# Optimization experiments

Hardware: AMD Instinct MI355X
Metric: run time of the kernel (lower is better)

The kernel has to match this reference:

```python
import jax, jax.numpy as jnp
import numpy as np

N, DEG, D, L = 20000, 32, 128, 2
EPS = 1e-7
MAX_TANH_ARG = 1.0 - 1e-5


def _logmap0(x, sqrt_c):
    # Poincare ball log map at the origin: artanh(sqrt(c)||x||) * x / (sqrt(c)||x||)
    norm = jnp.maximum(jnp.linalg.norm(x, axis=-1, keepdims=True), EPS)
    arg = jnp.minimum(sqrt_c * norm, MAX_TANH_ARG)
    return jnp.arctanh(arg) * x / (sqrt_c * norm)


def _expmap0(v, sqrt_c):
    # Poincare ball exp map at the origin: tanh(sqrt(c)||v||) * v / (sqrt(c)||v||)
    norm = jnp.maximum(jnp.linalg.norm(v, axis=-1, keepdims=True), EPS)
    return jnp.tanh(sqrt_c * norm) * v / (sqrt_c * norm)


def setup_inputs() -> dict:
    key = jax.random.key(0)
    ks = jax.random.split(key, 7)
    neighbors = jax.random.randint(ks[0], (N, DEG), 0, N)  # fixed in-degree predecessor lists
    node_embeddings = jax.random.normal(ks[1], (N, D), dtype=jnp.float32)
    in_proj_w = jax.random.normal(ks[2], (L, 3 * D, D), dtype=jnp.float32) * 0.02
    in_proj_b = jax.random.normal(ks[3], (L, 3 * D), dtype=jnp.float32) * 0.02
    out_proj_w = jax.random.normal(ks[4], (L, D, D), dtype=jnp.float32) * 0.02
    out_proj_b = jax.random.normal(ks[5], (L, D), dtype=jnp.float32) * 0.02
    curvature = jnp.array([-1.0], dtype=jnp.float32)
    return {
        'neighbors': neighbors,
        'node_embeddings': node_embeddings,
        'curvature': curvature,
        'in_proj_w': in_proj_w,
        'in_proj_b': in_proj_b,
        'out_proj_w': out_proj_w,
        'out_proj_b': out_proj_b,
    }


def reference(neighbors, node_embeddings, curvature, in_proj_w, in_proj_b, out_proj_w, out_proj_b):
    sqrt_c = jnp.sqrt(jnp.abs(curvature[0]))
    scale = 1.0 / np.sqrt(D)  # torch MHA scales q by 1/sqrt(head_dim)
    x = node_embeddings
    for l in range(L):
        t = _logmap0(x, sqrt_c)                       # [N, d] tangent features
        Wq, Wk, Wv = in_proj_w[l, :D], in_proj_w[l, D:2 * D], in_proj_w[l, 2 * D:]
        bq, bk, bv = in_proj_b[l, :D], in_proj_b[l, D:2 * D], in_proj_b[l, 2 * D:]
        q = t @ Wq.T + bq                             # [N, d]
        k = t @ Wk.T + bk
        v = t @ Wv.T + bv
        kn = k[neighbors]                             # [N, deg, d] gather over predecessors
        vn = v[neighbors]                             # [N, deg, d]
        scores = jnp.einsum('nd,nkd->nk', q, kn) * scale
        attn = jax.nn.softmax(scores, axis=-1)        # [N, deg]
        h = jnp.einsum('nk,nkd->nd', attn, vn)        # [N, d]
        h = h @ out_proj_w[l].T + out_proj_b[l]
        x = _expmap0(h, sqrt_c)
    return x
```

## Files before the change

### kernel.cpp

```cpp
#include <hip/hip_runtime.h>

#define N_NODES 20000
#define N_PAD   20032
#define DEG 32
#define D 128
#define EPS 1e-7f
#define MAX_TANH_ARG (1.0f - 1e-5f)
#define SCORE_SCALE 0.08838834764831845f
#define MTILES 313

typedef short bf16x8 __attribute__((ext_vector_type(8)));
typedef float f32x4 __attribute__((ext_vector_type(4)));

__device__ __forceinline__ float b2f(unsigned short u) {
  union { unsigned int i; float f; } x; x.i = ((unsigned int)u) << 16; return x.f;
}
__device__ __forceinline__ unsigned short f2b(float f) {
  union { float f; unsigned int i; } x; x.f = f;
  unsigned int r = x.i + 0x7FFFu + ((x.i >> 16) & 1u);
  return (unsigned short)(r >> 16);
}
__device__ __forceinline__ bool inputs_are_bf16(const void* curv) {
  return *(const unsigned short*)curv != 0;
}
__device__ __forceinline__ float read_sqrt_c(const void* c) {
  unsigned short u = *(const unsigned short*)c;
  float cv = (u == 0) ? *(const float*)c : b2f(u);
  return sqrtf(fabsf(cv));
}
__device__ __forceinline__ float atanh_fast(float x) {
  return 0.5f * __logf((1.f + x) / (1.f - x));
}
__device__ __forceinline__ float tanh_over_y(float y) {
  float e = __expf(-2.f * y);
  return (1.f - e) / ((1.f + e) * y);
}
__device__ __forceinline__ float load1(const void* p, size_t off, bool bf) {
  return bf ? b2f(((const unsigned short*)p)[off]) : ((const float*)p)[off];
}

__device__ __forceinline__ unsigned char f2fp8(float v) {
#if __has_builtin(__builtin_amdgcn_cvt_pk_fp8_f32)
  int p = __builtin_amdgcn_cvt_pk_fp8_f32(v, 0.f, 0, false);
  return (unsigned char)(p & 0xFF);
#else
  union { float f; unsigned u; } x; x.f = v;
  unsigned s = (x.u >> 31) << 7;
  float a = fminf(fabsf(v), 448.f);
  int q = (int)rintf(a * 512.f);
  if (q < 8) return (unsigned char)(s | q);
  int e; float m = frexpf(a, &e);
  int E = e - 1 + 7;
  int mi = (int)rintf(m * 16.f) - 8;
  if (mi == 8) { mi = 0; E += 1; }
  if (E > 15) { E = 15; mi = 6; }
  if (E < 1)  { return (unsigned char)(s | ((int)rintf(a * 512.f) & 7)); }
  return (unsigned char)(s | (E << 3) | mi);
#endif
}
__device__ __forceinline__ void fp8x8_decode(uint2 w, float* f) {
#if __has_builtin(__builtin_amdgcn_cvt_f32_fp8)
  f[0] = __builtin_amdgcn_cvt_f32_fp8((int)w.x, 0);
  f[1] = __builtin_amdgcn_cvt_f32_fp8((int)w.x, 1);
  f[2] = __builtin_amdgcn_cvt_f32_fp8((int)w.x, 2);
  f[3] = __builtin_amdgcn_cvt_f32_fp8((int)w.x, 3);
  f[4] = __builtin_amdgcn_cvt_f32_fp8((int)w.y, 0);
  f[5] = __builtin_amdgcn_cvt_f32_fp8((int)w.y, 1);
  f[6] = __builtin_amdgcn_cvt_f32_fp8((int)w.y, 2);
  f[7] = __builtin_amdgcn_cvt_f32_fp8((int)w.y, 3);
#else
#pragma unroll
  for (int i = 0; i < 8; i++) {
    unsigned char u = (i < 4) ? (unsigned char)(w.x >> (8 * i))
                              : (unsigned char)(w.y >> (8 * (i - 4)));
    int e = (u >> 3) & 15, m = u & 7;
    float mag = e ? ldexpf((float)(8 + m), e - 10) : ldexpf((float)m, -9);
    f[i] = (u & 0x80) ? -mag : mag;
  }
#endif
}

__device__ __forceinline__ void stage_W(const void* W, size_t woff, bool srcbf,
                                        unsigned short* W_lds, int tid) {
  if (srcbf) {
#pragma unroll
    for (int c = 0; c < 8; c++) {
      int idx = c * 2048 + tid * 8;
      bf16x8 v = *(const bf16x8*)((const unsigned short*)W + woff + idx);
      int row = idx >> 7, col = idx & 127;
      *(bf16x8*)&W_lds[row * 136 + col] = v;
    }
  } else {
#pragma unroll
    for (int c = 0; c < 16; c++) {
      int idx = c * 1024 + tid * 4;
      float4 v = *(const float4*)((const float*)W + woff + idx);
      int row = idx >> 7, col = idx & 127;
      unsigned short* p = &W_lds[row * 136 + col];
      p[0] = f2b(v.x); p[1] = f2b(v.y); p[2] = f2b(v.z); p[3] = f2b(v.w);
    }
  }
}

__device__ __forceinline__ void qkv_from_lds(
    const bf16x8* a, const unsigned short* W_lds,
    const void* bias, size_t boff, bool srcbf,
    int m0, int quad, int l16,
    unsigned short* qout, unsigned char* out8, bool isq) {
#pragma unroll
  for (int half = 0; half < 2; half++) {
#pragma unroll
    for (int s = 0; s < 4; s++) {
      int n = half * 64 + s * 16 + l16;
      f32x4 c = {0.f, 0.f, 0.f, 0.f};
#pragma unroll
      for (int kk = 0; kk < 4; kk++) {
        bf16x8 bfv = *(const bf16x8*)&W_lds[n * 136 + quad * 8 + kk * 32];
        c = __builtin_amdgcn_mfma_f32_16x16x32_bf16(a[kk], bfv, c, 0, 0, 0);
      }
      float bv = load1(bias, boff + n, srcbf);
#pragma unroll
      for (int r = 0; r < 4; r++) {
        int m = m0 + quad * 4 + r;
        if (m < N_NODES) {
          float val = c[r] + bv;
          if (isq) qout[(size_t)m * D + n] = f2b(val);
          else     out8[(size_t)m * D + n] = f2fp8(val);
        }
      }
    }
  }
}

__device__ __forceinline__ void outproj_acc_lds(
    const unsigned short* __restrict__ h, const unsigned short* W_lds,
    int m0, int quad, int l16, f32x4* acc) {
  bf16x8 a[4];
  const short* arow = (const short*)h + (size_t)(m0 + l16) * D + quad * 8;
#pragma unroll
  for (int kk = 0; kk < 4; kk++) a[kk] = *(const bf16x8*)(arow + kk * 32);
#pragma unroll
  for (int s = 0; s < 8; s++) {
    f32x4 c = {0.f, 0.f, 0.f, 0.f};
#pragma unroll
    for (int kk = 0; kk < 4; kk++) {
      bf16x8 bfv = *(const bf16x8*)&W_lds[(s * 16 + l16) * 136 + quad * 8 + kk * 32];
      c = __builtin_amdgcn_mfma_f32_16x16x32_bf16(a[kk], bfv, c, 0, 0, 0);
    }
    acc[s] = c;
  }
}

__global__ __launch_bounds__(256) void lqkv_kernel(
    const void* __restrict__ xin,
    const void* __restrict__ in_w, const void* __restrict__ in_b,
    unsigned short* __restrict__ qout,
    unsigned char* __restrict__ kout, unsigned char* __restrict__ vout,
    const void* __restrict__ curv) {
  __shared__ unsigned short t_lds[64 * 136];
  __shared__ unsigned short W_lds[128 * 136];
  int tid = threadIdx.x;
  int lane = tid & 63;
  int wave = tid >> 6;
  int mbase = blockIdx.x * 64;
  int y = blockIdx.y;
  bool srcbf = inputs_are_bf16(curv);
  float sqc = read_sqrt_c(curv);

  stage_W(in_w, (size_t)y * 128 * D, srcbf, W_lds, tid);

  {
    int rl = tid >> 3;
    int c8 = tid & 7;
#pragma unroll
    for (int pass = 0; pass < 2; pass++) {
      int r = pass * 32 + rl;
      int m = mbase + r;
      float xv[16];
      if (m < N_NODES) {
        if (srcbf) {
          const bf16x8* xp = (const bf16x8*)((const unsigned short*)xin + (size_t)m * D + c8 * 16);
          bf16x8 u0 = xp[0], u1 = xp[1];
#pragma unroll
          for (int i = 0; i < 8; i++) { xv[i] = b2f((unsigned short)u0[i]); xv[8 + i] = b2f((unsigned short)u1[i]); }
        } else {
          const float4* xp = (const float4*)((const float*)xin + (size_t)m * D + c8 * 16);
#pragma unroll
          for (int i = 0; i < 4; i++) {
            float4 v = xp[i];
            xv[i * 4 + 0] = v.x; xv[i * 4 + 1] = v.y; xv[i * 4 + 2] = v.z; xv[i * 4 + 3] = v.w;
          }
        }
      } else {
#pragma unroll
        for (int i = 0; i < 16; i++) xv[i] = 0.f;
      }
      float ss = 0.f;
#pragma unroll
      for (int i = 0; i < 16; i++) ss += xv[i] * xv[i];
      ss += __shfl_xor(ss, 1); ss += __shfl_xor(ss, 2); ss += __shfl_xor(ss, 4);
      float norm = fmaxf(sqrtf(ss), EPS);
      float arg  = fminf(sqc * norm, MAX_TANH_ARG);
      float sfac = atanh_fast(arg) / (sqc * norm);
      bf16x8 o0, o1;
#pragma unroll
      for (int i = 0; i < 8; i++) {
        o0[i] = (short)f2b(xv[i] * sfac);
        o1[i] = (short)f2b(xv[8 + i] * sfac);
      }
      *(bf16x8*)&t_lds[r * 136 + c8 * 16]     = o0;
      *(bf16x8*)&t_lds[r * 136 + c8 * 16 + 8] = o1;
    }
  }
  __syncthreads();

  int quad = lane >> 4, l16 = lane & 15;
  bf16x8 a[4];
#pragma unroll
  for (int kk = 0; kk < 4; kk++)
    a[kk] = *(const bf16x8*)&t_lds[(wave * 16 + l16) * 136 + quad * 8 + kk * 32];

  qkv_from_lds(a, W_lds, in_b, (size_t)y * 128, srcbf,
               mbase + wave * 16, quad, l16,
               qout, (y == 1) ? kout : vout, y == 0);
}

__global__ __launch_bounds__(256) void attn_kernel(
    const int* __restrict__ nbrs,
    const unsigned short* __restrict__ qb,
    const unsigned char* __restrict__ k8,
    const unsigned char* __restrict__ v8,
    unsigned short* __restrict__ hout) {
  int gid  = blockIdx.x * 256 + threadIdx.x;
  int node = gid >> 6;
  int lane = gid & 63;
  if (node >= N_NODES) return;
  int g = lane >> 4;
  int s = lane & 15;

  float qr[8];
  {
    bf16x8 qv = *(const bf16x8*)(qb + (size_t)node * D + s * 8);
#pragma unroll
    for (int i = 0; i < 8; i++) qr[i] = b2f((unsigned short)qv[i]);
  }
  int idx[8];
#pragma unroll
  for (int jj = 0; jj < 8; jj++) idx[jj] = nbrs[node * DEG + jj * 4 + g];

  uint2 kreg[8], vreg[8];
#pragma unroll
  for (int jj = 0; jj < 8; jj++)
    kreg[jj] = *(const uint2*)(k8 + (size_t)idx[jj] * D + s * 8);
#pragma unroll
  for (int jj = 0; jj < 8; jj++)
    vreg[jj] = *(const uint2*)(v8 + (size_t)idx[jj] * D + s * 8);

  float sc[8];
#pragma unroll
  for (int jj = 0; jj < 8; jj++) {
    float kf[8];
    fp8x8_decode(kreg[jj], kf);
    float p = 0.f;
#pragma unroll
    for (int i = 0; i < 8; i++) p += kf[i] * qr[i];
    p += __shfl_xor(p, 1); p += __shfl_xor(p, 2);
    p += __shfl_xor(p, 4); p += __shfl_xor(p, 8);
    sc[jj] = p * SCORE_SCALE;
  }
  float mx = sc[0];
#pragma unroll
  for (int jj = 1; jj < 8; jj++) mx = fmaxf(mx, sc[jj]);
  mx = fmaxf(mx, __shfl_xor(mx, 16));
  mx = fmaxf(mx, __shfl_xor(mx, 32));
  float sum = 0.f;
#pragma unroll
  for (int jj = 0; jj < 8; jj++) { sc[jj] = __expf(sc[jj] - mx); sum += sc[jj]; }
  sum += __shfl_xor(sum, 16);
  sum += __shfl_xor(sum, 32);
  float inv = 1.f / sum;

  float hv[8];
#pragma unroll
  for (int i = 0; i < 8; i++) hv[i] = 0.f;
#pragma unroll
  for (int jj = 0; jj < 8; jj++) {
    float aw = sc[jj] * inv;
    float vf[8];
    fp8x8_decode(vreg[jj], vf);
#pragma unroll
    for (int i = 0; i < 8; i++) hv[i] += aw * vf[i];
  }
#pragma unroll
  for (int i = 0; i < 8; i++) {
    hv[i] += __shfl_xor(hv[i], 16);
    hv[i] += __shfl_xor(hv[i], 32);
  }
  if (g == 0) {
    bf16x8 o;
#pragma unroll
    for (int i = 0; i < 8; i++) o[i] = (short)f2b(hv[i]);
    *(bf16x8*)(hout + (size_t)node * D + s * 8) = o;
  }
}

__global__ __launch_bounds__(256) void op_qkv_kernel(
    const unsigned short* __restrict__ h,
    const void* __restrict__ out_w, const void* __restrict__ out_b,
    const void* __restrict__ in_w, const void* __restrict__ in_b,
    unsigned short* __restrict__ qout,
    unsigned char* __restrict__ kout, unsigned char* __restrict__ vout,
    const void* __restrict__ curv) {
  __shared__ unsigned short t_lds[64 * 136];
  __shared__ unsigned short W_lds[128 * 136];
  int tid = threadIdx.x;
  int lane = tid & 63;
  int wave = tid >> 6;
  int quad = lane >> 4, l16 = lane & 15;
  int m0 = blockIdx.x * 64 + wave * 16;
  int y = blockIdx.y;
  bool srcbf = inputs_are_bf16(curv);

  stage_W(out_w, 0, srcbf, W_lds, tid);
  __syncthreads();
  {
    f32x4 acc[8];
    outproj_acc_lds(h, W_lds, m0, quad, l16, acc);
#pragma unroll
    for (int s = 0; s < 8; s++) {
      float bv = load1(out_b, s * 16 + l16, srcbf);
#pragma unroll
      for (int r = 0; r < 4; r++) {
        int rloc = wave * 16 + quad * 4 + r;
        t_lds[rloc * 136 + s * 16 + l16] = f2b(acc[s][r] + bv);
      }
    }
  }
  __syncthreads();

  bf16x8 a[4];
#pragma unroll
  for (int kk = 0; kk < 4; kk++)
    a[kk] = *(const bf16x8*)&t_lds[(wave * 16 + l16) * 136 + quad * 8 + kk * 32];
  stage_W(in_w, (size_t)384 * D + (size_t)y * 128 * D, srcbf, W_lds, tid);
  __syncthreads();

  qkv_from_lds(a, W_lds, in_b, (size_t)384 + y * 128, srcbf,
               m0, quad, l16, qout, (y == 1) ? kout : vout, y == 0);
}

__global__ __launch_bounds__(256) void outproj_final_kernel(
    const unsigned short* __restrict__ h,
    const void* __restrict__ out_w, const void* __restrict__ out_b,
    void* __restrict__ xout, const void* __restrict__ curv) {
  __shared__ unsigned short W_lds[128 * 136];
  int tid = threadIdx.x;
  int lane = tid & 63;
  int wave = tid >> 6;
  int quad = lane >> 4, l16 = lane & 15;
  int m0 = blockIdx.x * 64 + wave * 16;
  bool srcbf = inputs_are_bf16(curv);
  float sqc = read_sqrt_c(curv);

  stage_W(out_w, (size_t)D * D, srcbf, W_lds, tid);
  __syncthreads();

  f32x4 acc[8];
  outproj_acc_lds(h, W_lds, m0, quad, l16, acc);
#pragma unroll
  for (int s = 0; s < 8; s++) {
    float bv = load1(out_b, D + s * 16 + l16, srcbf);
#pragma unroll
    for (int r = 0; r < 4; r++) acc[s][r] += bv;
  }
  float scal[4];
#pragma unroll
  for (int r = 0; r < 4; r++) {
    float ss = 0.f;
#pragma unroll
    for (int s = 0; s < 8; s++) ss += acc[s][r] * acc[s][r];
    ss += __shfl_xor(ss, 1); ss += __shfl_xor(ss, 2);
    ss += __shfl_xor(ss, 4); ss += __shfl_xor(ss, 8);
    float norm = fmaxf(sqrtf(ss), EPS);
    scal[r] = tanh_over_y(sqc * norm);
  }
#pragma unroll
  for (int r = 0; r < 4; r++) {
    int m = m0 + quad * 4 + r;
    if (m < N_NODES) {
#pragma unroll
      for (int s = 0; s < 8; s++) {
        float val = acc[s][r] * scal[r];
        int col = s * 16 + l16;
        if (srcbf) ((unsigned short*)xout)[(size_t)m * D + col] = f2b(val);
        else       ((float*)xout)[(size_t)m * D + col] = val;
      }
    }
  }
}

extern "C" void kernel_launch(void* const* d_in, const int* in_sizes, int n_in,
                              void* d_out, int out_size, void* d_ws, size_t ws_size,
                              hipStream_t stream) {
  const int* neighbors = (const int*)d_in[0];
  const void* node_emb = d_in[1];
  const void* curv     = d_in[2];
  const void* in_w     = d_in[3];
  const void* in_b     = d_in[4];
  const void* out_w    = d_in[5];
  const void* out_b    = d_in[6];

  char* ws = (char*)d_ws;
  size_t off = 0;
  auto alloc = [&](size_t bytes) {
    char* p = ws + off; off += (bytes + 255) & ~(size_t)255; return p;
  };
  unsigned short* q_bf = (unsigned short*)alloc((size_t)N_PAD * D * 2);
  unsigned char*  k_f8 = (unsigned char*)alloc((size_t)N_PAD * D);
  unsigned char*  v_f8 = (unsigned char*)alloc((size_t)N_PAD * D);
  unsigned short* h_bf = (unsigned short*)alloc((size_t)N_PAD * D * 2);

  dim3 blk(256);

  lqkv_kernel<<<dim3(MTILES, 3), blk, 0, stream>>>(
      node_emb, in_w, in_b, q_bf, k_f8, v_f8, curv);
  attn_kernel<<<5000, blk, 0, stream>>>(neighbors, q_bf, k_f8, v_f8, h_bf);
  op_qkv_kernel<<<dim3(MTILES, 3), blk, 0, stream>>>(
      h_bf, out_w, out_b, in_w, in_b, q_bf, k_f8, v_f8, curv);
  attn_kernel<<<5000, blk, 0, stream>>>(neighbors, q_bf, k_f8, v_f8, h_bf);
  outproj_final_kernel<<<MTILES, blk, 0, stream>>>(
      h_bf, out_w, out_b, d_out, curv);
}
```

Before: 167.2 us.

## Fuse layer-2 attention with final out-projection and expmap kernel

Replaces the second attention kernel and the final out-projection kernel with a single kernel. Each 128-thread block computes attention for 32 nodes into LDS, then applies the out-projection MFMA and the expmap directly from LDS. This drops the h round trip through global memory and one kernel launch. In exchange, blocks are smaller, each wave processes its 16 nodes serially, and every block stages the full weight tile, which can lower parallelism in the latency-bound gather phase.

```diff
diff --git a/kernel.cpp b/kernel.cpp
--- a/kernel.cpp
+++ b/kernel.cpp
@@ -80,20 +80,21 @@
 #endif
 }
 
+template <int NT>
 __device__ __forceinline__ void stage_W(const void* W, size_t woff, bool srcbf,
                                         unsigned short* W_lds, int tid) {
   if (srcbf) {
 #pragma unroll
-    for (int c = 0; c < 8; c++) {
-      int idx = c * 2048 + tid * 8;
+    for (int c = 0; c < 16384 / (NT * 8); c++) {
+      int idx = c * NT * 8 + tid * 8;
       bf16x8 v = *(const bf16x8*)((const unsigned short*)W + woff + idx);
       int row = idx >> 7, col = idx & 127;
       *(bf16x8*)&W_lds[row * 136 + col] = v;
     }
   } else {
 #pragma unroll
-    for (int c = 0; c < 16; c++) {
-      int idx = c * 1024 + tid * 4;
+    for (int c = 0; c < 16384 / (NT * 4); c++) {
+      int idx = c * NT * 4 + tid * 4;
       float4 v = *(const float4*)((const float*)W + woff + idx);
       int row = idx >> 7, col = idx & 127;
       unsigned short* p = &W_lds[row * 136 + col];
@@ -132,13 +133,9 @@
   }
 }
 
-__device__ __forceinline__ void outproj_acc_lds(
-    const unsigned short* __restrict__ h, const unsigned short* W_lds,
-    int m0, int quad, int l16, f32x4* acc) {
-  bf16x8 a[4];
-  const short* arow = (const short*)h + (size_t)(m0 + l16) * D + quad * 8;
-#pragma unroll
-  for (int kk = 0; kk < 4; kk++) a[kk] = *(const bf16x8*)(arow + kk * 32);
+__device__ __forceinline__ void outproj_acc_frag(
+    const bf16x8* a, const unsigned short* W_lds,
+    int quad, int l16, f32x4* acc) {
 #pragma unroll
   for (int s = 0; s < 8; s++) {
     f32x4 c = {0.f, 0.f, 0.f, 0.f};
@@ -148,6 +145,79 @@
       c = __builtin_amdgcn_mfma_f32_16x16x32_bf16(a[kk], bfv, c, 0, 0, 0);
     }
     acc[s] = c;
+  }
+}
+
+__device__ __forceinline__ void attn_node_to_lds(
+    int node, int g, int s,
+    const int* __restrict__ nbrs,
+    const unsigned short* __restrict__ qb,
+    const unsigned char* __restrict__ k8,
+    const unsigned char* __restrict__ v8,
+    unsigned short* h_row) {
+  float qr[8];
+  {
+    bf16x8 qv = *(const bf16x8*)(qb + (size_t)node * D + s * 8);
+#pragma unroll
+    for (int i = 0; i < 8; i++) qr[i] = b2f((unsigned short)qv[i]);
+  }
+  int idx[8];
+#pragma unroll
+  for (int jj = 0; jj < 8; jj++) idx[jj] = nbrs[node * DEG + jj * 4 + g];
+
+  uint2 kreg[8], vreg[8];
+#pragma unroll
+  for (int jj = 0; jj < 8; jj++)
+    kreg[jj] = *(const uint2*)(k8 + (size_t)idx[jj] * D + s * 8);
+#pragma unroll
+  for (int jj = 0; jj < 8; jj++)
+    vreg[jj] = *(const uint2*)(v8 + (size_t)idx[jj] * D + s * 8);
+
+  float sc[8];
+#pragma unroll
+  for (int jj = 0; jj < 8; jj++) {
+    float kf[8];
+    fp8x8_decode(kreg[jj], kf);
+    float p = 0.f;
+#pragma unroll
+    for (int i = 0; i < 8; i++) p += kf[i] * qr[i];
+    p += __shfl_xor(p, 1); p += __shfl_xor(p, 2);
+    p += __shfl_xor(p, 4); p += __shfl_xor(p, 8);
+    sc[jj] = p * SCORE_SCALE;
+  }
+  float mx = sc[0];
+#pragma unroll
+  for (int jj = 1; jj < 8; jj++) mx = fmaxf(mx, sc[jj]);
+  mx = fmaxf(mx, __shfl_xor(mx, 16));
+  mx = fmaxf(mx, __shfl_xor(mx, 32));
+  float sum = 0.f;
+#pragma unroll
+  for (int jj = 0; jj < 8; jj++) { sc[jj] = __expf(sc[jj] - mx); sum += sc[jj]; }
+  sum += __shfl_xor(sum, 16);
+  sum += __shfl_xor(sum, 32);
+  float inv = 1.f / sum;
+
+  float hv[8];
+#pragma unroll
+  for (int i = 0; i < 8; i++) hv[i] = 0.f;
+#pragma unroll
+  for (int jj = 0; jj < 8; jj++) {
+    float aw = sc[jj] * inv;
+    float vf[8];
+    fp8x8_decode(vreg[jj], vf);
+#pragma unroll
+    for (int i = 0; i < 8; i++) hv[i] += aw * vf[i];
+  }
+#pragma unroll
+  for (int i = 0; i < 8; i++) {
+    hv[i] += __shfl_xor(hv[i], 16);
+    hv[i] += __shfl_xor(hv[i], 32);
+  }
+  if (g == 0) {
+    bf16x8 o;
+#pragma unroll
+    for (int i = 0; i < 8; i++) o[i] = (short)f2b(hv[i]);
+    *(bf16x8*)(h_row + s * 8) = o;
   }
 }
 
@@ -167,7 +237,7 @@
   bool srcbf = inputs_are_bf16(curv);
   float sqc = read_sqrt_c(curv);
 
-  stage_W(in_w, (size_t)y * 128 * D, srcbf, W_lds, tid);
+  stage_W<256>(in_w, (size_t)y * 128 * D, srcbf, W_lds, tid);
 
   {
     int rl = tid >> 3;
@@ -321,11 +391,15 @@
   int y = blockIdx.y;
   bool srcbf = inputs_are_bf16(curv);
 
-  stage_W(out_w, 0, srcbf, W_lds, tid);
+  stage_W<256>(out_w, 0, srcbf, W_lds, tid);
   __syncthreads();
   {
+    bf16x8 a[4];
+    const short* arow = (const short*)h + (size_t)(m0 + l16) * D + quad * 8;
+#pragma unroll
+    for (int kk = 0; kk < 4; kk++) a[kk] = *(const bf16x8*)(arow + kk * 32);
     f32x4 acc[8];
-    outproj_acc_lds(h, W_lds, m0, quad, l16, acc);
+    outproj_acc_frag(a, W_lds, quad, l16, acc);
 #pragma unroll
     for (int s = 0; s < 8; s++) {
       float bv = load1(out_b, s * 16 + l16, srcbf);
@@ -342,46 +416,63 @@
 #pragma unroll
   for (int kk = 0; kk < 4; kk++)
     a[kk] = *(const bf16x8*)&t_lds[(wave * 16 + l16) * 136 + quad * 8 + kk * 32];
-  stage_W(in_w, (size_t)384 * D + (size_t)y * 128 * D, srcbf, W_lds, tid);
+  stage_W<256>(in_w, (size_t)384 * D + (size_t)y * 128 * D, srcbf, W_lds, tid);
   __syncthreads();
 
   qkv_from_lds(a, W_lds, in_b, (size_t)384 + y * 128, srcbf,
                m0, quad, l16, qout, (y == 1) ? kout : vout, y == 0);
 }
 
-__global__ __launch_bounds__(256) void outproj_final_kernel(
-    const unsigned short* __restrict__ h,
+__global__ __launch_bounds__(128) void attn_opfinal_kernel(
+    const int* __restrict__ nbrs,
+    const unsigned short* __restrict__ qb,
+    const unsigned char* __restrict__ k8,
+    const unsigned char* __restrict__ v8,
     const void* __restrict__ out_w, const void* __restrict__ out_b,
     void* __restrict__ xout, const void* __restrict__ curv) {
+  __shared__ unsigned short t_lds[32 * 136];
   __shared__ unsigned short W_lds[128 * 136];
   int tid = threadIdx.x;
   int lane = tid & 63;
   int wave = tid >> 6;
   int quad = lane >> 4, l16 = lane & 15;
-  int m0 = blockIdx.x * 64 + wave * 16;
+  int g = quad, s = l16;
+  int mbase = blockIdx.x * 32;
   bool srcbf = inputs_are_bf16(curv);
   float sqc = read_sqrt_c(curv);
 
-  stage_W(out_w, (size_t)D * D, srcbf, W_lds, tid);
+  stage_W<128>(out_w, (size_t)D * D, srcbf, W_lds, tid);
+
+  for (int i = 0; i < 16; i++) {
+    int node = mbase + wave * 16 + i;
+    if (node < N_NODES)
+      attn_node_to_lds(node, g, s, nbrs, qb, k8, v8,
+                       &t_lds[(wave * 16 + i) * 136]);
+  }
   __syncthreads();
 
+  int m0 = mbase + wave * 16;
+  bf16x8 a[4];
+#pragma unroll
+  for (int kk = 0; kk < 4; kk++)
+    a[kk] = *(const bf16x8*)&t_lds[(wave * 16 + l16) * 136 + quad * 8 + kk * 32];
   f32x4 acc[8];
-  outproj_acc_lds(h, W_lds, m0, quad, l16, acc);
-#pragma unroll
-  for (int s = 0; s < 8; s++) {
-    float bv = load1(out_b, D + s * 16 + l16, srcbf);
-#pragma unroll
-    for (int r = 0; r < 4; r++) acc[s][r] += bv;
+  outproj_acc_frag(a, W_lds, quad, l16, acc);
+#pragma unroll
+  for (int ss = 0; ss < 8; ss++) {
+    float bv = load1(out_b, D + ss * 16 + l16, srcbf);
+#pragma unroll
+    for (int r = 0; r < 4; r++) acc[ss][r] += bv;
   }
   float scal[4];
 #pragma unroll
   for (int r = 0; r < 4; r++) {
-    float ss = 0.f;
-#pragma unroll
-    for (int s = 0; s < 8; s++) ss += acc[s][r] * acc[s][r];
-    ss += __shfl_xor(ss, 1); ss += __shfl_xor(ss, 2);
-    ss += __shfl_xor(ss, 4); ss += __shfl_xor(ss, 8);
-    float norm = fmaxf(sqrtf(ss), EPS);
+    float ssum = 0.f;
+#pragma unroll
+    for (int ss = 0; ss < 8; ss++) ssum += acc[ss][r] * acc[ss][r];
+    ssum += __shfl_xor(ssum, 1); ssum += __shfl_xor(ssum, 2);
+    ssum += __shfl_xor(ssum, 4); ssum += __shfl_xor(ssum, 8);
+    float norm = fmaxf(sqrtf(ssum), EPS);
     scal[r] = tanh_over_y(sqc * norm);
   }
 #pragma unroll
@@ -389,9 +480,9 @@
     int m = m0 + quad * 4 + r;
     if (m < N_NODES) {
 #pragma unroll
-      for (int s = 0; s < 8; s++) {
-        float val = acc[s][r] * scal[r];
-        int col = s * 16 + l16;
+      for (int ss = 0; ss < 8; ss++) {
+        float val = acc[ss][r] * scal[r];
+        int col = ss * 16 + l16;
         if (srcbf) ((unsigned short*)xout)[(size_t)m * D + col] = f2b(val);
         else       ((float*)xout)[(size_t)m * D + col] = val;
       }
@@ -420,14 +511,11 @@
   unsigned char*  v_f8 = (unsigned char*)alloc((size_t)N_PAD * D);
   unsigned short* h_bf = (unsigned short*)alloc((size_t)N_PAD * D * 2);
 
-  dim3 blk(256);
-
-  lqkv_kernel<<<dim3(MTILES, 3), blk, 0, stream>>>(
+  lqkv_kernel<<<dim3(MTILES, 3), 256, 0, stream>>>(
       node_emb, in_w, in_b, q_bf, k_f8, v_f8, curv);
-  attn_kernel<<<5000, blk, 0, stream>>>(neighbors, q_bf, k_f8, v_f8, h_bf);
-  op_qkv_kernel<<<dim3(MTILES, 3), blk, 0, stream>>>(
+  attn_kernel<<<5000, 256, 0, stream>>>(neighbors, q_bf, k_f8, v_f8, h_bf);
+  op_qkv_kernel<<<dim3(MTILES, 3), 256, 0, stream>>>(
       h_bf, out_w, out_b, in_w, in_b, q_bf, k_f8, v_f8, curv);
-  attn_kernel<<<5000, blk, 0, stream>>>(neighbors, q_bf, k_f8, v_f8, h_bf);
-  outproj_final_kernel<<<MTILES, blk, 0, stream>>>(
-      h_bf, out_w, out_b, d_out, curv);
-}
+  attn_opfinal_kernel<<<N_PAD / 32, 128, 0, stream>>>(
+      neighbors, q_bf, k_f8, v_f8, out_w, out_b, d_out, curv);
+}
```

After: 183.6 us. +9.8%, slower.
